# Performance work log

Hardware: AMD Instinct MI355X
Metric: run time of the kernel (lower is better)

Reference implementation:

```python
import jax, jax.numpy as jnp
import numpy as np

B, S, D, H = 2, 2048, 1024, 16
DH = D // H  # 64


def setup_inputs() -> dict:
    key = jax.random.key(0)
    ks = jax.random.split(key, 10)
    inp = {
        "q": jax.random.normal(ks[0], (B, S, D), jnp.float32),
        "k": jax.random.normal(ks[1], (B, S, D), jnp.float32),
        "v": jax.random.normal(ks[2], (B, S, D), jnp.float32),
        "mask": jax.random.randint(ks[3], (B, S), 0, 2, jnp.int32),
        "Wq": jax.random.normal(ks[4], (D, D), jnp.float32) * 0.02,
        "bq": jnp.zeros((D,), jnp.float32),
        "Wk": jax.random.normal(ks[5], (D, D), jnp.float32) * 0.02,
        "bk": jnp.zeros((D,), jnp.float32),
        "Wv": jax.random.normal(ks[6], (D, D), jnp.float32) * 0.02,
        "bv": jnp.zeros((D,), jnp.float32),
    }
    return inp


def _split_heads(x):
    # [B, S, D] -> [B, H, S, DH]
    b, s, _ = x.shape
    return x.reshape(b, s, H, DH).transpose(0, 2, 1, 3)


def reference(q, k, v, mask, Wq, bq, Wk, bk, Wv, bv):
    qh = _split_heads(q @ Wq + bq)
    kh = _split_heads(k @ Wk + bk)
    vh = _split_heads(v @ Wv + bv)
    # NOTE: original scales by sqrt(hidden_size), not sqrt(head_dim)
    scores = jnp.einsum("bhqd,bhkd->bhqk", qh, kh) / jnp.sqrt(jnp.float32(D))
    m = mask.astype(jnp.float32)[:, None, None, :]  # [B,1,1,S_k]
    scores = scores + (-1e9) * (1.0 - m)
    weights = jax.nn.softmax(scores, axis=-1)
    out = jnp.einsum("bhqk,bhkd->bhqd", weights, vh)
    # concat heads: [B,H,S,DH] -> [B,S,D]
    return out.transpose(0, 2, 1, 3).reshape(q.shape[0], -1, D)
```

## Files before the change

kernel.cpp:

```cpp
#include <hip/hip_runtime.h>


#define B_ 2
#define S_ 2048
#define D_ 1024
#define H_ 16
#define DH_ 64
#define M_ (B_*S_)

#define WT_OFF  ((size_t)3*4194304)
#define XB_OFF  (WT_OFF + (size_t)3*1048576)

typedef __attribute__((ext_vector_type(8))) short short8;
typedef __attribute__((ext_vector_type(4))) float f32x4;
typedef __attribute__((ext_vector_type(4))) unsigned int u32x4;
#define MFMA16(a,b,c) __builtin_amdgcn_mfma_f32_16x16x32_bf16(a,b,c,0,0,0)

typedef __attribute__((address_space(1))) const void* gptr_t;
typedef __attribute__((address_space(3))) void* lptr_t;
static __device__ inline void gload_lds16(const void* g, void* l) {
    __builtin_amdgcn_global_load_lds((gptr_t)g, (lptr_t)l, 16, 0, 0);
}

static __device__ inline unsigned short f2bf(float x) {
    union { float f; unsigned u; } v; v.f = x;
    return (unsigned short)((v.u + 0x7fffu + ((v.u >> 16) & 1u)) >> 16);
}
static __device__ inline unsigned packp(float a, float b) {
    return __builtin_amdgcn_perm(__float_as_uint(b) + 0x8000u,
                                 __float_as_uint(a) + 0x8000u, 0x07060302u);
}

__global__ __launch_bounds__(256) void convert_all(
    const float* __restrict__ X0, const float* __restrict__ X1,
    const float* __restrict__ X2,
    const float* __restrict__ Wq, const float* __restrict__ Wk,
    const float* __restrict__ Wv,
    unsigned short* __restrict__ O0, unsigned short* __restrict__ O1,
    unsigned short* __restrict__ O2, unsigned short* __restrict__ WtBase)
{
    __shared__ unsigned short T[64][72];
    const int z = blockIdx.z;
    const int t = threadIdx.x;

    if (blockIdx.x < 4096) {
        const float* X = z==0 ? X0 : (z==1 ? X1 : X2);
        unsigned short* O = z==0 ? O0 : (z==1 ? O1 : O2);
        int idx = blockIdx.x*256 + t;
        float4 xv = *(const float4*)&X[(size_t)idx*4];
        uint2 o;
        o.x = (unsigned)f2bf(xv.x) | ((unsigned)f2bf(xv.y) << 16);
        o.y = (unsigned)f2bf(xv.z) | ((unsigned)f2bf(xv.w) << 16);
        *(uint2*)&O[(size_t)idx*4] = o;
        return;
    }

    const float* W = z==0 ? Wq : (z==1 ? Wk : Wv);
    unsigned short* Out = WtBase + ((size_t)z << 20);
    const int bx2 = blockIdx.x - 4096;
    const int n0 = (bx2 & 15)*64, k0 = (bx2 >> 4)*64;
    const int tk = t >> 4, tn4 = (t & 15)*4;

    #pragma unroll
    for (int i=0;i<4;i++){
        int kk = tk + i*16;
        float4 wv = *(const float4*)&W[(size_t)(k0+kk)*D_ + n0 + tn4];
        T[tn4+0][kk] = f2bf(wv.x);
        T[tn4+1][kk] = f2bf(wv.y);
        T[tn4+2][kk] = f2bf(wv.z);
        T[tn4+3][kk] = f2bf(wv.w);
    }
    __syncthreads();

    const int n = t >> 2, seg = t & 3;
    uint4 a = *(uint4*)&T[n][seg*16];
    uint4 b = *(uint4*)&T[n][seg*16 + 8];
    *(uint4*)&Out[(size_t)(n0+n)*D_ + k0 + seg*16]     = a;
    *(uint4*)&Out[(size_t)(n0+n)*D_ + k0 + seg*16 + 8] = b;
}

__global__ __launch_bounds__(256) void proj_gemm(
    const unsigned short* __restrict__ A0, const unsigned short* __restrict__ A1,
    const unsigned short* __restrict__ A2, const unsigned short* __restrict__ WtBase,
    const float* __restrict__ b0, const float* __restrict__ b1,
    const float* __restrict__ b2, unsigned short* __restrict__ OutBase)
{
    const int which = blockIdx.z;
    const unsigned short* A  = which==0 ? A0 : (which==1 ? A1 : A2);
    const unsigned short* Bm = WtBase + ((size_t)which << 20);
    const float* bias        = which==0 ? b0 : (which==1 ? b1 : b2);
    unsigned short* Out      = OutBase + ((size_t)which << 22);
    const float oscale = (which==0) ? 0.04508422f : 1.0f;

    __shared__ __align__(16) unsigned short As[128*64];
    __shared__ __align__(16) unsigned short Bs[128*64];

    const int t    = threadIdx.x;
    const int m0   = blockIdx.y * 128;
    const int n0   = blockIdx.x * 128;
    const int w    = t >> 6;
    const int lane = t & 63;
    const int l15  = lane & 15;
    const int quad = lane >> 4;
    const int wm   = w >> 1, wn = w & 1;

    f32x4 acc[4][4];
    #pragma unroll
    for (int i=0;i<4;i++)
        #pragma unroll
        for (int j=0;j<4;j++) acc[i][j] = (f32x4){0.f,0.f,0.f,0.f};

    float biasv[4];
    #pragma unroll
    for (int nt=0; nt<4; nt++)
        biasv[nt] = bias[n0 + wn*64 + nt*16 + l15];

    int sArow[4], sAkc[4];
    #pragma unroll
    for (int i=0;i<4;i++){
        int s  = (w*4 + i)*64 + lane;
        int r  = s >> 3, cs = s & 7;
        sArow[i] = r;
        sAkc[i]  = ((cs ^ (r & 7)) * 8);
    }

    for (int ks = 0; ks < 16; ++ks) {
        const int kb = ks * 64;
        #pragma unroll
        for (int i=0;i<4;i++){
            int s = (w*4 + i)*64 + lane;
            gload_lds16(A  + (size_t)(m0 + sArow[i])*D_ + kb + sAkc[i], (unsigned short*)As + s*8);
            gload_lds16(Bm + (size_t)(n0 + sArow[i])*D_ + kb + sAkc[i], (unsigned short*)Bs + s*8);
        }
        __syncthreads();

        #pragma unroll
        for (int kh=0; kh<2; kh++){
            short8 aF[4], bF[4];
            #pragma unroll
            for (int mt=0; mt<4; mt++){
                int r  = wm*64 + mt*16 + l15;
                int cs = (kh*4 + quad) ^ (r & 7);
                aF[mt] = *(const short8*)(As + r*64 + cs*8);
            }
            #pragma unroll
            for (int nt=0; nt<4; nt++){
                int r  = wn*64 + nt*16 + l15;
                int cs = (kh*4 + quad) ^ (r & 7);
                bF[nt] = *(const short8*)(Bs + r*64 + cs*8);
            }
            #pragma unroll
            for (int mt=0; mt<4; mt++)
                #pragma unroll
                for (int nt=0; nt<4; nt++)
                    acc[mt][nt] = MFMA16(aF[mt], bF[nt], acc[mt][nt]);
        }
        __syncthreads();
    }

    if (which != 2) {
        #pragma unroll
        for (int nt=0; nt<4; nt++){
            int n  = n0 + wn*64 + nt*16 + l15;
            int hh = n >> 6, dh = n & 63;
            #pragma unroll
            for (int mt=0; mt<4; mt++){
                #pragma unroll
                for (int r=0; r<4; r++){
                    int m  = m0 + wm*64 + mt*16 + quad*4 + r;
                    int bb = m >> 11, ss = m & (S_-1);
                    float v = (acc[mt][nt][r] + biasv[nt]) * oscale;
                    Out[((size_t)((bb*H_ + hh)*S_ + ss))*DH_ + dh] = f2bf(v);
                }
            }
        }
    } else {
        #pragma unroll
        for (int nt=0; nt<4; nt++){
            int n  = n0 + wn*64 + nt*16 + l15;
            int hh = n >> 6, dh = n & 63;
            #pragma unroll
            for (int mt=0; mt<4; mt++){
                int m  = m0 + wm*64 + mt*16 + quad*4;
                int bb = m >> 11, ss = m & (S_-1);
                uint2 pk;
                pk.x = packp(acc[mt][nt][0] + biasv[nt], acc[mt][nt][1] + biasv[nt]);
                pk.y = packp(acc[mt][nt][2] + biasv[nt], acc[mt][nt][3] + biasv[nt]);
                *(uint2*)&Out[((size_t)((bb*H_ + hh)*DH_ + dh))*S_ + ss] = pk;
            }
        }
    }
}

__global__ __launch_bounds__(256, 2) void attn_kernel(
    const unsigned short* __restrict__ ws, const int* __restrict__ mask,
    float* __restrict__ out)
{
    const unsigned short* Qh = ws;
    const unsigned short* Kh = ws + (size_t)M_*D_;
    const unsigned short* Vg = ws + 2*(size_t)M_*D_;

    const int lin = blockIdx.x + (blockIdx.y << 4) + (blockIdx.z << 8);
    const int Wn  = (lin & 7)*64 + (lin >> 3);
    const int qt = Wn & 15;
    const int h  = (Wn >> 4) & 15;
    const int bb = Wn >> 8;

    const size_t base = ((size_t)(bb*H_ + h)) * S_ * DH_;
    const int q0 = qt * 128;

    __shared__ __align__(16) unsigned char smem[34816];
    unsigned short* KsB = (unsigned short*)smem;
    unsigned short* VtB = (unsigned short*)(smem + 16384);
    float*          MsB = (float*)(smem + 32768);
    float*          Ob  = (float*)smem;

    const int t    = threadIdx.x;
    const int w    = t >> 6;
    const int lane = t & 63;
    const int l15  = lane & 15;
    const int quad = lane >> 4;

    short8 qf[2][2];
    #pragma unroll
    for (int qs=0; qs<2; qs++){
        const unsigned short* qp = Qh + base + (size_t)(q0 + w*32 + qs*16 + l15)*DH_ + quad*8;
        qf[qs][0] = *(const short8*)(qp);
        qf[qs][1] = *(const short8*)(qp + 32);
    }

    f32x4 accO[2][4];
    #pragma unroll
    for (int qs=0; qs<2; qs++)
        #pragma unroll
        for (int i=0;i<4;i++) accO[qs][i] = (f32x4){0.f,0.f,0.f,0.f};
    float l_run[2] = {0.f, 0.f};

    int rr[2], cc[2], ssl[2], gK[2];
    #pragma unroll
    for (int i=0;i<2;i++){
        int s = (w*2 + i)*64 + lane;
        int r = s >> 3, cs = s & 7;
        ssl[i] = s;
        rr[i]  = r;
        cc[i]  = (cs ^ (r & 7)) * 8;
        gK[i]  = ((r >> 4) & 1)*32 + ((r >> 2) & 3)*8 + (r >> 5)*4 + (r & 3);
    }

    #define ISSUE(k0v, p) do {                                                 \
        _Pragma("unroll")                                                      \
        for (int i=0;i<2;i++){                                                 \
            gload_lds16(Kh + base + (size_t)((k0v) + gK[i])*DH_ + cc[i],       \
                        KsB + (p)*4096 + ssl[i]*8);                            \
            gload_lds16(Vg + base + (size_t)rr[i]*S_ + (k0v) + cc[i],          \
                        VtB + (p)*4096 + ssl[i]*8);                            \
        }                                                                      \
    } while(0)

    ISSUE(0, 0);
    if (t < 64) MsB[t] = mask[bb*S_ + t] ? 0.f : -1e9f;
    __syncthreads();

    for (int it = 0; it < 32; ++it){
        const int p = it & 1;
        int mR = 0;
        if (it < 31){
            ISSUE((it+1)*64, 1-p);
            if (t < 64) mR = mask[bb*S_ + (it+1)*64 + t];
        }
        const unsigned short* Ks  = KsB + p*4096;
        const unsigned short* Vts = VtB + p*4096;
        const float* Ms = MsB + p*64;

        f32x4 msv[4];
        #pragma unroll
        for (int st=0; st<4; st++)
            msv[st] = *(const f32x4*)&Ms[(st&1)*32 + (st>>1)*4 + quad*8];

        short8 ka[4], kb[4];
        #pragma unroll
        for (int st=0; st<4; st++){
            int row = st*16 + l15;
            const unsigned short* kr = Ks + row*64;
            ka[st] = *(const short8*)(kr + ((quad    ) ^ (row & 7))*8);
            kb[st] = *(const short8*)(kr + ((quad + 4) ^ (row & 7))*8);
        }
        short8 vf[4][2];
        #pragma unroll
        for (int mt=0; mt<4; mt++){
            int row = mt*16 + l15;
            const unsigned short* vr = Vts + row*64;
            vf[mt][0] = *(const short8*)(vr + ((quad    ) ^ (row & 7))*8);
            vf[mt][1] = *(const short8*)(vr + ((quad + 4) ^ (row & 7))*8);
        }

        #pragma unroll
        for (int qs=0; qs<2; qs++){
            f32x4 sc[4];
            #pragma unroll
            for (int st=0; st<4; st++){
                f32x4 a = (f32x4){0.f,0.f,0.f,0.f};
                a = MFMA16(ka[st], qf[qs][0], a);
                a = MFMA16(kb[st], qf[qs][1], a);
                sc[st] = a;
            }
            float pv[4][4]; float lacc = 0.f;
            #pragma unroll
            for (int st=0; st<4; st++)
                #pragma unroll
                for (int rj=0; rj<4; rj++){
                    pv[st][rj] = __builtin_amdgcn_exp2f(sc[st][rj] + msv[st][rj]);
                    lacc += pv[st][rj];
                }
            l_run[qs] += lacc;
            u32x4 u0 = { packp(pv[0][0],pv[0][1]), packp(pv[0][2],pv[0][3]),
                         packp(pv[2][0],pv[2][1]), packp(pv[2][2],pv[2][3]) };
            u32x4 u1 = { packp(pv[1][0],pv[1][1]), packp(pv[1][2],pv[1][3]),
                         packp(pv[3][0],pv[3][1]), packp(pv[3][2],pv[3][3]) };
            short8 pf0 = __builtin_bit_cast(short8, u0);
            short8 pf1 = __builtin_bit_cast(short8, u1);
            #pragma unroll
            for (int mt=0; mt<4; mt++){
                accO[qs][mt] = MFMA16(vf[mt][0], pf0, accO[qs][mt]);
                accO[qs][mt] = MFMA16(vf[mt][1], pf1, accO[qs][mt]);
            }
        }

        if (it < 31 && t < 64) MsB[(1-p)*64 + t] = mR ? 0.f : -1e9f;
        __syncthreads();
    }

    #pragma unroll
    for (int qs=0; qs<2; qs++){
        float l = l_run[qs];
        l += __shfl_xor(l, 16);
        l += __shfl_xor(l, 32);
        float invl = 1.0f / fmaxf(l, 1e-30f);
        #pragma unroll
        for (int mt=0; mt<4; mt++)
            #pragma unroll
            for (int r=0; r<4; r++)
                Ob[(w*32 + qs*16 + l15)*68 + mt*16 + quad*4 + r] = accO[qs][mt][r]*invl;
    }
    __syncthreads();

    #pragma unroll
    for (int i=0;i<8;i++){
        int f  = (i*256 + t)*4;
        int qq = f >> 6, dh = f & 63;
        float4 o = *(float4*)&Ob[qq*68 + dh];
        *(float4*)&out[((size_t)(bb*S_ + q0 + qq))*D_ + h*DH_ + dh] = o;
    }
    #undef ISSUE
}

extern "C" void kernel_launch(void* const* d_in, const int* in_sizes, int n_in,
                              void* d_out, int out_size, void* d_ws, size_t ws_size,
                              hipStream_t stream) {
    const float* q    = (const float*)d_in[0];
    const float* k    = (const float*)d_in[1];
    const float* v    = (const float*)d_in[2];
    const int*   mask = (const int*)d_in[3];
    const float* Wq   = (const float*)d_in[4];
    const float* b0   = (const float*)d_in[5];
    const float* Wk   = (const float*)d_in[6];
    const float* b1   = (const float*)d_in[7];
    const float* Wv   = (const float*)d_in[8];
    const float* b2   = (const float*)d_in[9];
    float* out = (float*)d_out;
    unsigned short* ws = (unsigned short*)d_ws;

    unsigned short* xq = ws + XB_OFF;
    unsigned short* xk = (unsigned short*)d_out;
    unsigned short* xv = (unsigned short*)d_out + 4194304;

    convert_all<<<dim3(4352,1,3), 256, 0, stream>>>(q, k, v, Wq, Wk, Wv,
                                                    xq, xk, xv, ws + WT_OFF);
    proj_gemm<<<dim3(8,32,3), 256, 0, stream>>>(xq, xk, xv, ws + WT_OFF,
                                                b0, b1, b2, ws);
    attn_kernel<<<dim3(16,16,2), 256, 0, stream>>>(ws, mask, out);
}
```

Measured before the change: 206.3 us.

## Double K/V tile to 128 keys, preload full mask, fold mask into MFMA accumulator

The attention loop now stages 128-key K/V tiles per iteration (16 iterations instead of 32), so half as many block-wide barriers are needed. The whole per-batch mask row is converted into LDS once up front, which removes the per-iteration mask fetch. The mask bias now seeds the QK^T MFMA accumulator instead of being added afterwards, and row sums are kept as vectors. s_setprio hints are added around the MFMA sections. LDS use grows from about 34KB to 72KB per block, which may cut occupancy below the two blocks per CU requested by launch bounds.

```diff
diff --git a/kernel.cpp b/kernel.cpp
--- a/kernel.cpp
+++ b/kernel.cpp
@@ -209,10 +209,10 @@
     const size_t base = ((size_t)(bb*H_ + h)) * S_ * DH_;
     const int q0 = qt * 128;
 
-    __shared__ __align__(16) unsigned char smem[34816];
+    __shared__ __align__(16) unsigned char smem[73728];
     unsigned short* KsB = (unsigned short*)smem;
-    unsigned short* VtB = (unsigned short*)(smem + 16384);
-    float*          MsB = (float*)(smem + 32768);
+    unsigned short* VtB = (unsigned short*)(smem + 32768);
+    float*          MsT = (float*)(smem + 65536);
     float*          Ob  = (float*)smem;
 
     const int t    = threadIdx.x;
@@ -234,105 +234,113 @@
     for (int qs=0; qs<2; qs++)
         #pragma unroll
         for (int i=0;i<4;i++) accO[qs][i] = (f32x4){0.f,0.f,0.f,0.f};
-    float l_run[2] = {0.f, 0.f};
-
-    int rr[2], cc[2], ssl[2], gK[2];
-    #pragma unroll
-    for (int i=0;i<2;i++){
-        int s = (w*2 + i)*64 + lane;
-        int r = s >> 3, cs = s & 7;
+    f32x4 lv[2] = {(f32x4){0.f,0.f,0.f,0.f}, (f32x4){0.f,0.f,0.f,0.f}};
+
+    int rr[4], cc[4], ssl[4], gK[4];
+    #pragma unroll
+    for (int i=0;i<4;i++){
+        int s  = (w*4 + i)*64 + lane;
+        int r  = s >> 3, cs = s & 7;
+        int r6 = r & 63;
         ssl[i] = s;
         rr[i]  = r;
         cc[i]  = (cs ^ (r & 7)) * 8;
-        gK[i]  = ((r >> 4) & 1)*32 + ((r >> 2) & 3)*8 + (r >> 5)*4 + (r & 3);
-    }
-
-    #define ISSUE(k0v, p) do {                                                 \
+        gK[i]  = (r & 64) + ((r6 >> 4) & 1)*32 + ((r6 >> 2) & 3)*8 + (r6 >> 5)*4 + (r6 & 3);
+    }
+
+    #define ISSUE128(k0v, p) do {                                              \
         _Pragma("unroll")                                                      \
-        for (int i=0;i<2;i++){                                                 \
+        for (int i=0;i<4;i++){                                                 \
             gload_lds16(Kh + base + (size_t)((k0v) + gK[i])*DH_ + cc[i],       \
-                        KsB + (p)*4096 + ssl[i]*8);                            \
-            gload_lds16(Vg + base + (size_t)rr[i]*S_ + (k0v) + cc[i],          \
-                        VtB + (p)*4096 + ssl[i]*8);                            \
+                        KsB + (p)*8192 + ssl[i]*8);                            \
+            gload_lds16(Vg + base + (size_t)(rr[i] & 63)*S_ + (k0v)            \
+                            + (rr[i] & 64) + cc[i],                            \
+                        VtB + (p)*8192 + ssl[i]*8);                            \
         }                                                                      \
     } while(0)
 
-    ISSUE(0, 0);
-    if (t < 64) MsB[t] = mask[bb*S_ + t] ? 0.f : -1e9f;
+    ISSUE128(0, 0);
+    #pragma unroll
+    for (int i=0;i<8;i++){
+        int idx = i*256 + t;
+        MsT[idx] = mask[bb*S_ + idx] ? 0.f : -1e9f;
+    }
     __syncthreads();
 
-    for (int it = 0; it < 32; ++it){
+    for (int it = 0; it < 16; ++it){
         const int p = it & 1;
-        int mR = 0;
-        if (it < 31){
-            ISSUE((it+1)*64, 1-p);
-            if (t < 64) mR = mask[bb*S_ + (it+1)*64 + t];
-        }
-        const unsigned short* Ks  = KsB + p*4096;
-        const unsigned short* Vts = VtB + p*4096;
-        const float* Ms = MsB + p*64;
-
-        f32x4 msv[4];
-        #pragma unroll
-        for (int st=0; st<4; st++)
-            msv[st] = *(const f32x4*)&Ms[(st&1)*32 + (st>>1)*4 + quad*8];
-
-        short8 ka[4], kb[4];
-        #pragma unroll
-        for (int st=0; st<4; st++){
-            int row = st*16 + l15;
-            const unsigned short* kr = Ks + row*64;
-            ka[st] = *(const short8*)(kr + ((quad    ) ^ (row & 7))*8);
-            kb[st] = *(const short8*)(kr + ((quad + 4) ^ (row & 7))*8);
-        }
-        short8 vf[4][2];
-        #pragma unroll
-        for (int mt=0; mt<4; mt++){
-            int row = mt*16 + l15;
-            const unsigned short* vr = Vts + row*64;
-            vf[mt][0] = *(const short8*)(vr + ((quad    ) ^ (row & 7))*8);
-            vf[mt][1] = *(const short8*)(vr + ((quad + 4) ^ (row & 7))*8);
-        }
-
-        #pragma unroll
-        for (int qs=0; qs<2; qs++){
-            f32x4 sc[4];
+        if (it < 15) ISSUE128((it+1)*128, 1-p);
+
+        #pragma unroll
+        for (int sb = 0; sb < 2; ++sb){
+            const unsigned short* Ks  = KsB + p*8192 + sb*4096;
+            const unsigned short* Vts = VtB + p*8192 + sb*4096;
+            const float*          Mp  = MsT + it*128 + sb*64;
+
+            f32x4 msv[4];
+            #pragma unroll
+            for (int st=0; st<4; st++)
+                msv[st] = *(const f32x4*)&Mp[(st&1)*32 + (st>>1)*4 + quad*8];
+
+            short8 ka[4], kb[4];
             #pragma unroll
             for (int st=0; st<4; st++){
-                f32x4 a = (f32x4){0.f,0.f,0.f,0.f};
-                a = MFMA16(ka[st], qf[qs][0], a);
-                a = MFMA16(kb[st], qf[qs][1], a);
-                sc[st] = a;
-            }
-            float pv[4][4]; float lacc = 0.f;
-            #pragma unroll
-            for (int st=0; st<4; st++)
-                #pragma unroll
-                for (int rj=0; rj<4; rj++){
-                    pv[st][rj] = __builtin_amdgcn_exp2f(sc[st][rj] + msv[st][rj]);
-                    lacc += pv[st][rj];
+                int row = st*16 + l15;
+                const unsigned short* kr = Ks + row*64;
+                ka[st] = *(const short8*)(kr + ((quad    ) ^ (row & 7))*8);
+                kb[st] = *(const short8*)(kr + ((quad + 4) ^ (row & 7))*8);
+            }
+            short8 vf[4][2];
+            #pragma unroll
+            for (int mt=0; mt<4; mt++){
+                int row = mt*16 + l15;
+                const unsigned short* vr = Vts + row*64;
+                vf[mt][0] = *(const short8*)(vr + ((quad    ) ^ (row & 7))*8);
+                vf[mt][1] = *(const short8*)(vr + ((quad + 4) ^ (row & 7))*8);
+            }
+
+            #pragma unroll
+            for (int qs=0; qs<2; qs++){
+                f32x4 sc[4];
+                __builtin_amdgcn_s_setprio(1);
+                #pragma unroll
+                for (int st=0; st<4; st++){
+                    f32x4 a = msv[st];
+                    a = MFMA16(ka[st], qf[qs][0], a);
+                    a = MFMA16(kb[st], qf[qs][1], a);
+                    sc[st] = a;
                 }
-            l_run[qs] += lacc;
-            u32x4 u0 = { packp(pv[0][0],pv[0][1]), packp(pv[0][2],pv[0][3]),
-                         packp(pv[2][0],pv[2][1]), packp(pv[2][2],pv[2][3]) };
-            u32x4 u1 = { packp(pv[1][0],pv[1][1]), packp(pv[1][2],pv[1][3]),
-                         packp(pv[3][0],pv[3][1]), packp(pv[3][2],pv[3][3]) };
-            short8 pf0 = __builtin_bit_cast(short8, u0);
-            short8 pf1 = __builtin_bit_cast(short8, u1);
-            #pragma unroll
-            for (int mt=0; mt<4; mt++){
-                accO[qs][mt] = MFMA16(vf[mt][0], pf0, accO[qs][mt]);
-                accO[qs][mt] = MFMA16(vf[mt][1], pf1, accO[qs][mt]);
-            }
-        }
-
-        if (it < 31 && t < 64) MsB[(1-p)*64 + t] = mR ? 0.f : -1e9f;
+                __builtin_amdgcn_s_setprio(0);
+                f32x4 pvv[4];
+                #pragma unroll
+                for (int st=0; st<4; st++)
+                    #pragma unroll
+                    for (int rj=0; rj<4; rj++)
+                        pvv[st][rj] = __builtin_amdgcn_exp2f(sc[st][rj]);
+                f32x4 s01 = pvv[0] + pvv[1];
+                f32x4 s23 = pvv[2] + pvv[3];
+                lv[qs] += (s01 + s23);
+                u32x4 u0 = { packp(pvv[0][0],pvv[0][1]), packp(pvv[0][2],pvv[0][3]),
+                             packp(pvv[2][0],pvv[2][1]), packp(pvv[2][2],pvv[2][3]) };
+                u32x4 u1 = { packp(pvv[1][0],pvv[1][1]), packp(pvv[1][2],pvv[1][3]),
+                             packp(pvv[3][0],pvv[3][1]), packp(pvv[3][2],pvv[3][3]) };
+                short8 pf0 = __builtin_bit_cast(short8, u0);
+                short8 pf1 = __builtin_bit_cast(short8, u1);
+                __builtin_amdgcn_s_setprio(1);
+                #pragma unroll
+                for (int mt=0; mt<4; mt++){
+                    accO[qs][mt] = MFMA16(vf[mt][0], pf0, accO[qs][mt]);
+                    accO[qs][mt] = MFMA16(vf[mt][1], pf1, accO[qs][mt]);
+                }
+                __builtin_amdgcn_s_setprio(0);
+            }
+        }
         __syncthreads();
     }
 
     #pragma unroll
     for (int qs=0; qs<2; qs++){
-        float l = l_run[qs];
+        float l = (lv[qs][0] + lv[qs][1]) + (lv[qs][2] + lv[qs][3]);
         l += __shfl_xor(l, 16);
         l += __shfl_xor(l, 32);
         float invl = 1.0f / fmaxf(l, 1e-30f);
@@ -351,7 +359,7 @@
         float4 o = *(float4*)&Ob[qq*68 + dh];
         *(float4*)&out[((size_t)(bb*S_ + q0 + qq))*D_ + h*DH_ + dh] = o;
     }
-    #undef ISSUE
+    #undef ISSUE128
 }
 
 extern "C" void kernel_launch(void* const* d_in, const int* in_sizes, int n_in,
```

Result: faster. 202.2 us (-2.0%).
